# Kernel optimization log

Hardware: AMD Instinct MI355X
Metric: run time of the kernel (lower is better)

Reference implementation:

```python
import jax, jax.numpy as jnp
import numpy as np

B, S, H = 2, 2048, 1024          # batch, seq, hidden_size
I = 512                          # expert_ffn_hidden_size
E_R, E_Z = 32, 8                 # routed experts, zero (identity) experts
E_T = E_R + E_Z                  # total experts
K = 6                            # moe_topk
SCALE = 2.5                      # routed_scaling_factor
W_INIT = 0.02


def setup_inputs() -> dict:
    key = jax.random.key(0)
    k0, k1, k2, k3 = jax.random.split(key, 4)
    return {
        "hidden_states": jax.random.normal(k0, (B, S, H), jnp.float32),
        "classifier_weight": jax.random.normal(k1, (E_T, H), jnp.float32) * W_INIT,
        "e_score_correction_bias": jnp.zeros((E_T,), jnp.float32),
        "gate_up_proj": jax.random.normal(k2, (E_T, 2 * I, H), jnp.float32) * W_INIT,
        "down_proj": jax.random.normal(k3, (E_R, H, I), jnp.float32) * W_INIT,
    }


def reference(hidden_states, classifier_weight, e_score_correction_bias,
              gate_up_proj, down_proj):
    orig_shape = hidden_states.shape
    x = hidden_states.reshape(-1, H).astype(jnp.float32)      # [T, H]
    T = x.shape[0]

    # ---- router (fp32 like the torch code) ----
    logits = x @ classifier_weight.T                          # [T, E_T]
    scores = jax.nn.softmax(logits, axis=-1)
    _, topk_idx = jax.lax.top_k(scores + e_score_correction_bias[None, :], K)
    topk_w = jnp.take_along_axis(scores, topk_idx, axis=1) * SCALE  # [T, K]

    # dense per-(token, expert) combine weights; 0 for unselected experts
    w_full = jnp.zeros((T, E_T), jnp.float32).at[
        jnp.arange(T)[:, None], topk_idx].add(topk_w)          # [T, E_T]

    # zero experts: weighted identity
    zero_w = w_full[:, E_R:].sum(axis=-1, keepdims=True)       # [T, 1]
    out0 = x * zero_w

    # routed experts: SwiGLU MLP per expert, scanned over experts
    routed_w = w_full[:, :E_R].T                               # [E_R, T]

    def body(out, xs):
        Wgu, Wd, we = xs                                       # [2I,H],[H,I],[T]
        gate, up = jnp.split(x @ Wgu.T, 2, axis=-1)            # [T, I] each
        y = (jax.nn.silu(gate) * up) @ Wd.T                    # [T, H]
        return out + we[:, None] * y, None

    out, _ = jax.lax.scan(body, out0, (gate_up_proj[:E_R], down_proj, routed_w))
    return out.reshape(orig_shape).astype(hidden_states.dtype)
```

## Files before the change

kernel.cpp:

```cpp
#include <hip/hip_runtime.h>
#include <float.h>
#include <math.h>

#define TT 4096
#define HH 1024
#define II 512
#define E_R 32
#define E_T 40
#define TOPK 6
#define SCALE_F 2.5f
#define MAXTILES 224

typedef __bf16 bf16x8 __attribute__((ext_vector_type(8)));
typedef float f32x4 __attribute__((ext_vector_type(4)));

__device__ inline unsigned short f2bf(float f) {
  __bf16 h = (__bf16)f;
  return __builtin_bit_cast(unsigned short, h);
}

__device__ inline bf16x8 cvt8v(float4 a, float4 b) {
  bf16x8 v;
  v[0] = (__bf16)a.x; v[1] = (__bf16)a.y; v[2] = (__bf16)a.z; v[3] = (__bf16)a.w;
  v[4] = (__bf16)b.x; v[5] = (__bf16)b.y; v[6] = (__bf16)b.z; v[7] = (__bf16)b.w;
  return v;
}

__device__ inline void gload_lds16(const void* g, void* l) {
  __builtin_amdgcn_global_load_lds(
      (__attribute__((address_space(1))) void*)g,
      (__attribute__((address_space(3))) void*)l, 16, 0, 0);
}

__device__ inline bf16x8 lds_frag(const unsigned short* base, int row, int kb) {
  int byte = (row * 128 + kb * 2) ^ ((row & 7) << 4);
  uint4 v = *reinterpret_cast<const uint4*>(reinterpret_cast<const char*>(base) + byte);
  return __builtin_bit_cast(bf16x8, v);
}

__device__ inline bf16x8 lds_frag_f32(const float* base, int row, int kb) {
  int key = row & 15;
  int c0 = (kb >> 2) ^ key;
  int c1 = ((kb >> 2) + 1) ^ key;
  const char* p = reinterpret_cast<const char*>(base) + row * 256;
  float4 lo = *reinterpret_cast<const float4*>(p + c0 * 16);
  float4 hi = *reinterpret_cast<const float4*>(p + c1 * 16);
  return cvt8v(lo, hi);
}

__device__ inline f32x4 mfma16(bf16x8 a, bf16x8 b, f32x4 c) {
  return __builtin_amdgcn_mfma_f32_16x16x32_bf16(a, b, c, 0, 0, 0);
}

__global__ __launch_bounds__(256) void k_logits(const float* __restrict__ x,
                                                const float* __restrict__ wcls,
                                                float* __restrict__ logits,
                                                unsigned short* __restrict__ xb) {
  __shared__ float4 ws4[E_T * 64];
  const int tid = threadIdx.x;
  const int lane = tid & 63;
  const int wave = tid >> 6;
  const int token = blockIdx.x * 4 + wave;
  const float4* x4 = reinterpret_cast<const float4*>(x);
  const float4* w4 = reinterpret_cast<const float4*>(wcls);

  float acc[E_T];
  #pragma unroll
  for (int e = 0; e < E_T; ++e) acc[e] = 0.f;

  for (int c = 0; c < 4; ++c) {
    if (c) __syncthreads();
    #pragma unroll
    for (int j = 0; j < 10; ++j) {
      int v = tid + j * 256;
      int e = v >> 6, kq = v & 63;
      ws4[v] = w4[e * 256 + c * 64 + kq];
    }
    float4 xv = x4[(size_t)token * 256 + c * 64 + lane];
    ushort4 s;
    s.x = f2bf(xv.x); s.y = f2bf(xv.y); s.z = f2bf(xv.z); s.w = f2bf(xv.w);
    reinterpret_cast<ushort4*>(xb + (size_t)token * HH)[c * 64 + lane] = s;
    __syncthreads();
    #pragma unroll
    for (int e = 0; e < E_T; ++e) {
      float4 w = ws4[e * 64 + lane];
      acc[e] += xv.x * w.x + xv.y * w.y + xv.z * w.z + xv.w * w.w;
    }
  }

  float mine = 0.f;
  #pragma unroll
  for (int e = 0; e < E_T; ++e) {
    float r = acc[e];
    #pragma unroll
    for (int o = 32; o; o >>= 1) r += __shfl_xor(r, o);
    if (lane == e) mine = r;
  }
  if (lane < E_T) logits[(size_t)token * E_T + lane] = mine;
}

__global__ void k_topk(const float* __restrict__ logits, const float* __restrict__ bias,
                       float* __restrict__ zero_w, int* __restrict__ counts,
                       int* __restrict__ tok_list,
                       int* __restrict__ route_ep, float* __restrict__ route_w,
                       int* __restrict__ route_n) {
  int t = blockIdx.x * 64 + threadIdx.x;
  float l[E_T];
  const float4* lp = reinterpret_cast<const float4*>(logits + (size_t)t * E_T);
  #pragma unroll
  for (int j = 0; j < E_T / 4; ++j) {
    float4 v = lp[j];
    l[j * 4 + 0] = v.x; l[j * 4 + 1] = v.y; l[j * 4 + 2] = v.z; l[j * 4 + 3] = v.w;
  }
  float m = -FLT_MAX;
  #pragma unroll
  for (int e = 0; e < E_T; ++e) m = fmaxf(m, l[e]);
  float den = 0.f;
  #pragma unroll
  for (int e = 0; e < E_T; ++e) { l[e] = __expf(l[e] - m); den += l[e]; }
  float inv = 1.f / den;
  float sel[E_T];
  #pragma unroll
  for (int e = 0; e < E_T; ++e) { l[e] *= inv; sel[e] = l[e] + bias[e]; }

  unsigned long long used = 0ull;
  float zw = 0.f;
  int nr = 0;
  for (int k = 0; k < TOPK; ++k) {
    float bv = -FLT_MAX; int bj = 0;
    #pragma unroll
    for (int e = 0; e < E_T; ++e) {
      float v = ((used >> e) & 1ull) ? -FLT_MAX : sel[e];
      if (v > bv) { bv = v; bj = e; }
    }
    used |= 1ull << bj;
    float wgt = (bv - bias[bj]) * SCALE_F;
    if (bj >= E_R) {
      zw += wgt;
    } else {
      int p = atomicAdd(&counts[bj], 1);
      tok_list[bj * TT + p] = t;
      route_ep[t * TOPK + nr] = (bj << 16) | p;
      route_w[t * TOPK + nr] = wgt;
      nr++;
    }
  }
  zero_w[t] = zw;
  route_n[t] = nr;
}

__global__ void k_scan(const int* __restrict__ counts, int* __restrict__ offsets,
                       int* __restrict__ tiles) {
  if (threadIdx.x == 0) {
    int s = 0, idx = 0;
    for (int e = 0; e < E_R; ++e) {
      offsets[e] = s;
      int c = counts[e];
      s += c;
      for (int r0 = 0; r0 < c; r0 += 128) tiles[1 + idx++] = (e << 16) | r0;
    }
    offsets[E_R] = s;
    tiles[0] = idx;
  }
}

__global__ __launch_bounds__(256, 3) void k_gemm1(
    const unsigned short* __restrict__ xb, const float* __restrict__ gup,
    const int* __restrict__ tok_list, const int* __restrict__ counts,
    const int* __restrict__ offsets, const int* __restrict__ tiles,
    unsigned short* __restrict__ inter) {
  const int nt = tiles[0];
  if ((int)blockIdx.y >= nt) return;
  const int tv = tiles[1 + blockIdx.y];
  const int e = tv >> 16;
  const int row0 = tv & 0xffff;
  const int cnt = counts[e];
  const int off = offsets[e];
  const int n0 = blockIdx.x * 64;
  const int tid = threadIdx.x;
  const int lane = tid & 63;
  const int wave = tid >> 6;
  const int wr = wave >> 1;
  const int wc = wave & 1;

  __shared__ __align__(16) unsigned short lA[128 * 64];
  __shared__ __align__(16) float lBg[64 * 64];
  __shared__ __align__(16) float lBu[64 * 64];
  __shared__ int toks[128];

  if (tid < 128) {
    int r = row0 + tid;
    toks[tid] = tok_list[e * TT + (r < cnt ? r : cnt - 1)];
  }
  __syncthreads();

  unsigned aoff[4];
  #pragma unroll
  for (int i = 0; i < 4; ++i) {
    int lrow = wave * 32 + i * 8 + (lane >> 3);
    aoff[i] = (unsigned)toks[lrow] * HH + (((lane & 7) ^ (lrow & 7)) * 8);
  }
  const float* gbase = gup + (size_t)e * 1024 * HH;
  unsigned boff[4];
  #pragma unroll
  for (int i = 0; i < 4; ++i) {
    int rt = wave * 16 + i * 4 + (lane >> 4);
    boff[i] = (unsigned)(n0 + rt) * HH + (((lane & 15) ^ (rt & 15)) * 4);
  }
  const unsigned upjump = 512u * HH;

  f32x4 accg[4][2] = {}; f32x4 accu[4][2] = {};

  for (int k0 = 0; k0 < HH; k0 += 64) {
    #pragma unroll
    for (int i = 0; i < 4; ++i)
      gload_lds16(xb + aoff[i] + k0, lA + (wave * 32 + i * 8) * 64);
    #pragma unroll
    for (int i = 0; i < 4; ++i) {
      gload_lds16(gbase + boff[i] + k0,          lBg + (wave * 16 + i * 4) * 64);
      gload_lds16(gbase + boff[i] + upjump + k0, lBu + (wave * 16 + i * 4) * 64);
    }
    __syncthreads();
    #pragma unroll
    for (int ks = 0; ks < 2; ++ks) {
      int kb = ks * 32 + ((lane >> 4) << 3);
      bf16x8 a[4], g[2], u[2];
      #pragma unroll
      for (int i = 0; i < 4; ++i) a[i] = lds_frag(lA, wr * 64 + i * 16 + (lane & 15), kb);
      #pragma unroll
      for (int j = 0; j < 2; ++j) {
        g[j] = lds_frag_f32(lBg, wc * 32 + j * 16 + (lane & 15), kb);
        u[j] = lds_frag_f32(lBu, wc * 32 + j * 16 + (lane & 15), kb);
      }
      #pragma unroll
      for (int i = 0; i < 4; ++i)
        #pragma unroll
        for (int j = 0; j < 2; ++j) {
          accg[i][j] = mfma16(a[i], g[j], accg[i][j]);
          accu[i][j] = mfma16(a[i], u[j], accu[i][j]);
        }
    }
    __syncthreads();
  }

  #pragma unroll
  for (int i = 0; i < 4; ++i)
    #pragma unroll
    for (int j = 0; j < 2; ++j)
      #pragma unroll
      for (int r = 0; r < 4; ++r) {
        int rloc = wr * 64 + i * 16 + ((lane >> 4) << 2) + r;
        int grow = row0 + rloc;
        if (grow < cnt) {
          int col = n0 + wc * 32 + j * 16 + (lane & 15);
          float gv = accg[i][j][r], uv = accu[i][j][r];
          float act = gv / (1.f + __expf(-gv)) * uv;
          inter[(size_t)(off + grow) * II + col] = f2bf(act);
        }
      }
}

__global__ __launch_bounds__(256, 3) void k_gemm2(
    const unsigned short* __restrict__ inter, const float* __restrict__ dwn,
    const int* __restrict__ counts, const int* __restrict__ offsets,
    const int* __restrict__ tiles, unsigned short* __restrict__ inter2) {
  const int nt = tiles[0];
  if ((int)blockIdx.y >= nt) return;
  const int tv = tiles[1 + blockIdx.y];
  const int e = tv >> 16;
  const int row0 = tv & 0xffff;
  const int cnt = counts[e];
  const int off = offsets[e];
  const int h0 = blockIdx.x * 128;
  const int tid = threadIdx.x;
  const int lane = tid & 63;
  const int wave = tid >> 6;
  const int wr = wave >> 1;
  const int wc = wave & 1;

  __shared__ __align__(16) unsigned short lA[128 * 64];
  __shared__ __align__(16) float lB[128 * 64];

  unsigned aoff[4];
  #pragma unroll
  for (int i = 0; i < 4; ++i) {
    int lrow = wave * 32 + i * 8 + (lane >> 3);
    int rr = row0 + lrow; rr = rr < cnt ? rr : cnt - 1;
    aoff[i] = (unsigned)(off + rr) * II + (((lane & 7) ^ (lrow & 7)) * 8);
  }
  const float* dbase = dwn + (size_t)e * HH * II;
  unsigned boff[8];
  #pragma unroll
  for (int i = 0; i < 8; ++i) {
    int rt = wave * 32 + i * 4 + (lane >> 4);
    boff[i] = (unsigned)(h0 + rt) * II + (((lane & 15) ^ (rt & 15)) * 4);
  }

  f32x4 acc[4][4] = {};

  for (int k0 = 0; k0 < II; k0 += 64) {
    #pragma unroll
    for (int i = 0; i < 4; ++i)
      gload_lds16(inter + aoff[i] + k0, lA + (wave * 32 + i * 8) * 64);
    #pragma unroll
    for (int i = 0; i < 8; ++i)
      gload_lds16(dbase + boff[i] + k0, lB + (wave * 32 + i * 4) * 64);
    __syncthreads();
    #pragma unroll
    for (int ks = 0; ks < 2; ++ks) {
      int kb = ks * 32 + ((lane >> 4) << 3);
      bf16x8 a[4], b[4];
      #pragma unroll
      for (int i = 0; i < 4; ++i) a[i] = lds_frag(lA, wr * 64 + i * 16 + (lane & 15), kb);
      #pragma unroll
      for (int j = 0; j < 4; ++j) b[j] = lds_frag_f32(lB, wc * 64 + j * 16 + (lane & 15), kb);
      #pragma unroll
      for (int i = 0; i < 4; ++i)
        #pragma unroll
        for (int j = 0; j < 4; ++j)
          acc[i][j] = mfma16(a[i], b[j], acc[i][j]);
    }
    __syncthreads();
  }

  #pragma unroll
  for (int i = 0; i < 4; ++i)
    #pragma unroll
    for (int j = 0; j < 4; ++j)
      #pragma unroll
      for (int r = 0; r < 4; ++r) {
        int rloc = wr * 64 + i * 16 + ((lane >> 4) << 2) + r;
        int grow = row0 + rloc;
        if (grow < cnt) {
          int h = h0 + wc * 64 + j * 16 + (lane & 15);
          inter2[(size_t)(off + grow) * HH + h] = f2bf(acc[i][j][r]);
        }
      }
}

__global__ __launch_bounds__(256) void k_combine(
    const float* __restrict__ x, const float* __restrict__ zero_w,
    const int* __restrict__ offsets, const int* __restrict__ route_ep,
    const float* __restrict__ route_w, const int* __restrict__ route_n,
    const unsigned short* __restrict__ inter2, float* __restrict__ out) {
  const int t = blockIdx.x;
  const int tid = threadIdx.x;
  const float zw = zero_w[t];
  const int n = route_n[t];
  float4 o = reinterpret_cast<const float4*>(x)[t * 256 + tid];
  o.x *= zw; o.y *= zw; o.z *= zw; o.w *= zw;
  for (int i = 0; i < n; ++i) {
    int ep = route_ep[t * TOPK + i];
    int row = offsets[ep >> 16] + (ep & 0xffff);
    float w = route_w[t * TOPK + i];
    ushort4 v = reinterpret_cast<const ushort4*>(inter2 + (size_t)row * HH)[tid];
    o.x += w * __builtin_bit_cast(float, (unsigned)v.x << 16);
    o.y += w * __builtin_bit_cast(float, (unsigned)v.y << 16);
    o.z += w * __builtin_bit_cast(float, (unsigned)v.z << 16);
    o.w += w * __builtin_bit_cast(float, (unsigned)v.w << 16);
  }
  reinterpret_cast<float4*>(out)[t * 256 + tid] = o;
}


extern "C" void kernel_launch(void* const* d_in, const int* in_sizes, int n_in,
                              void* d_out, int out_size, void* d_ws, size_t ws_size,
                              hipStream_t stream) {
  const float* x    = (const float*)d_in[0];
  const float* wcls = (const float*)d_in[1];
  const float* bias = (const float*)d_in[2];
  const float* gup  = (const float*)d_in[3];
  const float* dwn  = (const float*)d_in[4];
  float* out = (float*)d_out;

  char* w = (char*)d_ws;
  unsigned short* xb    = (unsigned short*)(w + 0);
  float* zero_w         = (float*)(w + 8388608);
  int* counts           = (int*)(w + 8404992);
  int* offsets          = (int*)(w + 8405120);
  int* tok_list         = (int*)(w + 8405376);
  float* logits         = (float*)(w + 8929664);
  int* tiles            = (int*)(w + 9585024);
  int* route_ep         = (int*)(w + 9589120);
  float* route_w        = (float*)(w + 9687424);
  int* route_n          = (int*)(w + 9785728);
  unsigned short* inter = (unsigned short*)(w + 9802112);
  unsigned short* inter2 = (unsigned short*)(w + 34967936);

  hipMemsetAsync(counts, 0, E_R * sizeof(int), stream);
  k_logits<<<1024, 256, 0, stream>>>(x, wcls, logits, xb);
  k_topk<<<64, 64, 0, stream>>>(logits, bias, zero_w, counts, tok_list,
                                route_ep, route_w, route_n);
  k_scan<<<1, 64, 0, stream>>>(counts, offsets, tiles);
  k_gemm1<<<dim3(8, MAXTILES), 256, 0, stream>>>(xb, gup, tok_list, counts, offsets, tiles, inter);
  k_gemm2<<<dim3(8, MAXTILES), 256, 0, stream>>>(inter, dwn, counts, offsets, tiles, inter2);
  k_combine<<<TT, 256, 0, stream>>>(x, zero_w, offsets, route_ep, route_w, route_n,
                                    inter2, out);
}
```

Measured before the change: 227.3 us.

## Pre-convert expert weights to bf16 and double-buffer LDS in expert GEMMs

Adds a kernel that converts the routed gate/up and down weights from fp32 to bf16 into workspace on every call. Both grouped GEMMs then stream bf16 weights through the same swizzled bf16 fragment path as activations, removing the per-fragment fp32-to-bf16 conversion and halving weight bytes loaded per tile. The K loops are also reorganised into two-stage LDS double buffering so the next tile's loads overlap the current MFMAs. In exchange the conversion pass adds roughly 190MB of reads and 96MB of writes per call, and LDS use per block grows, which may lower occupancy below the requested three blocks per CU.

```diff
diff --git a/kernel.cpp b/kernel.cpp
--- a/kernel.cpp
+++ b/kernel.cpp
@@ -10,6 +10,8 @@
 #define TOPK 6
 #define SCALE_F 2.5f
 #define MAXTILES 224
+#define NGUP (32*1024*1024)
+#define NDWN (32*1024*512)
 
 typedef __bf16 bf16x8 __attribute__((ext_vector_type(8)));
 typedef float f32x4 __attribute__((ext_vector_type(4)));
@@ -38,18 +40,20 @@
   return __builtin_bit_cast(bf16x8, v);
 }
 
-__device__ inline bf16x8 lds_frag_f32(const float* base, int row, int kb) {
-  int key = row & 15;
-  int c0 = (kb >> 2) ^ key;
-  int c1 = ((kb >> 2) + 1) ^ key;
-  const char* p = reinterpret_cast<const char*>(base) + row * 256;
-  float4 lo = *reinterpret_cast<const float4*>(p + c0 * 16);
-  float4 hi = *reinterpret_cast<const float4*>(p + c1 * 16);
-  return cvt8v(lo, hi);
-}
-
 __device__ inline f32x4 mfma16(bf16x8 a, bf16x8 b, f32x4 c) {
   return __builtin_amdgcn_mfma_f32_16x16x32_bf16(a, b, c, 0, 0, 0);
+}
+
+__global__ __launch_bounds__(256) void k_convert_w(const float* __restrict__ gup,
+                                                   const float* __restrict__ dwn,
+                                                   uint4* __restrict__ wb) {
+  unsigned i = blockIdx.x * 256 + threadIdx.x;
+  const unsigned NGq = NGUP / 8;
+  const float4* src = (i < NGq)
+      ? reinterpret_cast<const float4*>(gup) + (size_t)i * 2
+      : reinterpret_cast<const float4*>(dwn) + (size_t)(i - NGq) * 2;
+  float4 a = src[0], b = src[1];
+  wb[i] = __builtin_bit_cast(uint4, cvt8v(a, b));
 }
 
 __global__ __launch_bounds__(256) void k_logits(const float* __restrict__ x,
@@ -165,7 +169,7 @@
 }
 
 __global__ __launch_bounds__(256, 3) void k_gemm1(
-    const unsigned short* __restrict__ xb, const float* __restrict__ gup,
+    const unsigned short* __restrict__ xb, const unsigned short* __restrict__ gupb,
     const int* __restrict__ tok_list, const int* __restrict__ counts,
     const int* __restrict__ offsets, const int* __restrict__ tiles,
     unsigned short* __restrict__ inter) {
@@ -183,9 +187,9 @@
   const int wr = wave >> 1;
   const int wc = wave & 1;
 
-  __shared__ __align__(16) unsigned short lA[128 * 64];
-  __shared__ __align__(16) float lBg[64 * 64];
-  __shared__ __align__(16) float lBu[64 * 64];
+  __shared__ __align__(16) unsigned short lA[2][128 * 64];
+  __shared__ __align__(16) unsigned short lBg[2][64 * 64];
+  __shared__ __align__(16) unsigned short lBu[2][64 * 64];
   __shared__ int toks[128];
 
   if (tid < 128) {
@@ -200,37 +204,50 @@
     int lrow = wave * 32 + i * 8 + (lane >> 3);
     aoff[i] = (unsigned)toks[lrow] * HH + (((lane & 7) ^ (lrow & 7)) * 8);
   }
-  const float* gbase = gup + (size_t)e * 1024 * HH;
-  unsigned boff[4];
-  #pragma unroll
-  for (int i = 0; i < 4; ++i) {
-    int rt = wave * 16 + i * 4 + (lane >> 4);
-    boff[i] = (unsigned)(n0 + rt) * HH + (((lane & 15) ^ (rt & 15)) * 4);
+  const unsigned short* gb = gupb + (size_t)e * (1024 * HH);
+  unsigned boff[2];
+  #pragma unroll
+  for (int i = 0; i < 2; ++i) {
+    int lrow = wave * 16 + i * 8 + (lane >> 3);
+    boff[i] = (unsigned)(n0 + lrow) * HH + (((lane & 7) ^ (lrow & 7)) * 8);
   }
   const unsigned upjump = 512u * HH;
 
   f32x4 accg[4][2] = {}; f32x4 accu[4][2] = {};
 
-  for (int k0 = 0; k0 < HH; k0 += 64) {
-    #pragma unroll
-    for (int i = 0; i < 4; ++i)
-      gload_lds16(xb + aoff[i] + k0, lA + (wave * 32 + i * 8) * 64);
-    #pragma unroll
-    for (int i = 0; i < 4; ++i) {
-      gload_lds16(gbase + boff[i] + k0,          lBg + (wave * 16 + i * 4) * 64);
-      gload_lds16(gbase + boff[i] + upjump + k0, lBu + (wave * 16 + i * 4) * 64);
-    }
-    __syncthreads();
+#define G1_STAGE(T, B)                                                          \
+  {                                                                             \
+    int k0s = (T) * 64;                                                         \
+    _Pragma("unroll")                                                           \
+    for (int i = 0; i < 4; ++i)                                                 \
+      gload_lds16(xb + aoff[i] + k0s, lA[B] + (wave * 32 + i * 8) * 64);        \
+    _Pragma("unroll")                                                           \
+    for (int i = 0; i < 2; ++i) {                                               \
+      gload_lds16(gb + boff[i] + k0s,          lBg[B] + (wave * 16 + i * 8) * 64); \
+      gload_lds16(gb + boff[i] + upjump + k0s, lBu[B] + (wave * 16 + i * 8) * 64); \
+    }                                                                           \
+  }
+
+  G1_STAGE(0, 0);
+  __syncthreads();
+
+  for (int t = 0; t < 16; ++t) {
+    if (t < 15) {
+      if ((t + 1) & 1) { G1_STAGE(t + 1, 1); } else { G1_STAGE(t + 1, 0); }
+    }
+    const unsigned short* cA  = (t & 1) ? lA[1]  : lA[0];
+    const unsigned short* cBg = (t & 1) ? lBg[1] : lBg[0];
+    const unsigned short* cBu = (t & 1) ? lBu[1] : lBu[0];
     #pragma unroll
     for (int ks = 0; ks < 2; ++ks) {
       int kb = ks * 32 + ((lane >> 4) << 3);
       bf16x8 a[4], g[2], u[2];
       #pragma unroll
-      for (int i = 0; i < 4; ++i) a[i] = lds_frag(lA, wr * 64 + i * 16 + (lane & 15), kb);
+      for (int i = 0; i < 4; ++i) a[i] = lds_frag(cA, wr * 64 + i * 16 + (lane & 15), kb);
       #pragma unroll
       for (int j = 0; j < 2; ++j) {
-        g[j] = lds_frag_f32(lBg, wc * 32 + j * 16 + (lane & 15), kb);
-        u[j] = lds_frag_f32(lBu, wc * 32 + j * 16 + (lane & 15), kb);
+        g[j] = lds_frag(cBg, wc * 32 + j * 16 + (lane & 15), kb);
+        u[j] = lds_frag(cBu, wc * 32 + j * 16 + (lane & 15), kb);
       }
       #pragma unroll
       for (int i = 0; i < 4; ++i)
@@ -261,7 +278,7 @@
 }
 
 __global__ __launch_bounds__(256, 3) void k_gemm2(
-    const unsigned short* __restrict__ inter, const float* __restrict__ dwn,
+    const unsigned short* __restrict__ inter, const unsigned short* __restrict__ dwnb,
     const int* __restrict__ counts, const int* __restrict__ offsets,
     const int* __restrict__ tiles, unsigned short* __restrict__ inter2) {
   const int nt = tiles[0];
@@ -278,8 +295,8 @@
   const int wr = wave >> 1;
   const int wc = wave & 1;
 
-  __shared__ __align__(16) unsigned short lA[128 * 64];
-  __shared__ __align__(16) float lB[128 * 64];
+  __shared__ __align__(16) unsigned short lA[2][128 * 64];
+  __shared__ __align__(16) unsigned short lB[2][128 * 64];
 
   unsigned aoff[4];
   #pragma unroll
@@ -288,32 +305,44 @@
     int rr = row0 + lrow; rr = rr < cnt ? rr : cnt - 1;
     aoff[i] = (unsigned)(off + rr) * II + (((lane & 7) ^ (lrow & 7)) * 8);
   }
-  const float* dbase = dwn + (size_t)e * HH * II;
-  unsigned boff[8];
-  #pragma unroll
-  for (int i = 0; i < 8; ++i) {
-    int rt = wave * 32 + i * 4 + (lane >> 4);
-    boff[i] = (unsigned)(h0 + rt) * II + (((lane & 15) ^ (rt & 15)) * 4);
+  const unsigned short* db = dwnb + (size_t)e * (HH * II);
+  unsigned boff[4];
+  #pragma unroll
+  for (int i = 0; i < 4; ++i) {
+    int lrow = wave * 32 + i * 8 + (lane >> 3);
+    boff[i] = (unsigned)(h0 + lrow) * II + (((lane & 7) ^ (lrow & 7)) * 8);
   }
 
   f32x4 acc[4][4] = {};
 
-  for (int k0 = 0; k0 < II; k0 += 64) {
-    #pragma unroll
-    for (int i = 0; i < 4; ++i)
-      gload_lds16(inter + aoff[i] + k0, lA + (wave * 32 + i * 8) * 64);
-    #pragma unroll
-    for (int i = 0; i < 8; ++i)
-      gload_lds16(dbase + boff[i] + k0, lB + (wave * 32 + i * 4) * 64);
-    __syncthreads();
+#define G2_STAGE(T, B)                                                          \
+  {                                                                             \
+    int k0s = (T) * 64;                                                         \
+    _Pragma("unroll")                                                           \
+    for (int i = 0; i < 4; ++i)                                                 \
+      gload_lds16(inter + aoff[i] + k0s, lA[B] + (wave * 32 + i * 8) * 64);     \
+    _Pragma("unroll")                                                           \
+    for (int i = 0; i < 4; ++i)                                                 \
+      gload_lds16(db + boff[i] + k0s, lB[B] + (wave * 32 + i * 8) * 64);        \
+  }
+
+  G2_STAGE(0, 0);
+  __syncthreads();
+
+  for (int t = 0; t < 8; ++t) {
+    if (t < 7) {
+      if ((t + 1) & 1) { G2_STAGE(t + 1, 1); } else { G2_STAGE(t + 1, 0); }
+    }
+    const unsigned short* cA = (t & 1) ? lA[1] : lA[0];
+    const unsigned short* cB = (t & 1) ? lB[1] : lB[0];
     #pragma unroll
     for (int ks = 0; ks < 2; ++ks) {
       int kb = ks * 32 + ((lane >> 4) << 3);
       bf16x8 a[4], b[4];
       #pragma unroll
-      for (int i = 0; i < 4; ++i) a[i] = lds_frag(lA, wr * 64 + i * 16 + (lane & 15), kb);
-      #pragma unroll
-      for (int j = 0; j < 4; ++j) b[j] = lds_frag_f32(lB, wc * 64 + j * 16 + (lane & 15), kb);
+      for (int i = 0; i < 4; ++i) a[i] = lds_frag(cA, wr * 64 + i * 16 + (lane & 15), kb);
+      #pragma unroll
+      for (int j = 0; j < 4; ++j) b[j] = lds_frag(cB, wc * 64 + j * 16 + (lane & 15), kb);
       #pragma unroll
       for (int i = 0; i < 4; ++i)
         #pragma unroll
@@ -386,14 +415,17 @@
   int* route_n          = (int*)(w + 9785728);
   unsigned short* inter = (unsigned short*)(w + 9802112);
   unsigned short* inter2 = (unsigned short*)(w + 34967936);
+  unsigned short* gupb  = (unsigned short*)(w + 85299584);
+  unsigned short* dwnb  = (unsigned short*)(w + 152408448);
 
   hipMemsetAsync(counts, 0, E_R * sizeof(int), stream);
+  k_convert_w<<<(NGUP + NDWN) / 8 / 256, 256, 0, stream>>>(gup, dwn, (uint4*)gupb);
   k_logits<<<1024, 256, 0, stream>>>(x, wcls, logits, xb);
   k_topk<<<64, 64, 0, stream>>>(logits, bias, zero_w, counts, tok_list,
                                 route_ep, route_w, route_n);
   k_scan<<<1, 64, 0, stream>>>(counts, offsets, tiles);
-  k_gemm1<<<dim3(8, MAXTILES), 256, 0, stream>>>(xb, gup, tok_list, counts, offsets, tiles, inter);
-  k_gemm2<<<dim3(8, MAXTILES), 256, 0, stream>>>(inter, dwn, counts, offsets, tiles, inter2);
+  k_gemm1<<<dim3(8, MAXTILES), 256, 0, stream>>>(xb, gupb, tok_list, counts, offsets, tiles, inter);
+  k_gemm2<<<dim3(8, MAXTILES), 256, 0, stream>>>(inter, dwnb, counts, offsets, tiles, inter2);
   k_combine<<<TT, 256, 0, stream>>>(x, zero_w, offsets, route_ep, route_w, route_n,
                                     inter2, out);
 }
```

New measurement: 262.9 us. +15.7%, slower.
